# Kernel tuning notes

Hardware: AMD Instinct MI355X
Metric: run time of the kernel (lower is better)

## Reference

```python
import jax, jax.numpy as jnp
import numpy as np

BS, Q, K, NT = 16, 1500, 256, 150   # batch, queries, classes, GT per image (T = BS*NT)
COST_CLASS, COST_BBOX, COST_GIOU = 1.0, 5.0, 2.0
ALPHA, GAMMA, EPS = 0.25, 2.0, 1e-8


def box_cxcywh_to_xyxy(b):
    cx, cy, w, h = b[..., 0], b[..., 1], b[..., 2], b[..., 3]
    return jnp.stack([cx - 0.5 * w, cy - 0.5 * h, cx + 0.5 * w, cy + 0.5 * h], axis=-1)


def generalized_box_iou(boxes1, boxes2):
    # boxes in xyxy; boxes1: [N,4], boxes2: [M,4] -> [N,M]
    area1 = (boxes1[:, 2] - boxes1[:, 0]) * (boxes1[:, 3] - boxes1[:, 1])
    area2 = (boxes2[:, 2] - boxes2[:, 0]) * (boxes2[:, 3] - boxes2[:, 1])
    lt = jnp.maximum(boxes1[:, None, :2], boxes2[None, :, :2])
    rb = jnp.minimum(boxes1[:, None, 2:], boxes2[None, :, 2:])
    wh = jnp.clip(rb - lt, 0.0)
    inter = wh[..., 0] * wh[..., 1]
    union = area1[:, None] + area2[None, :] - inter
    iou = inter / union
    # smallest enclosing box
    lt_e = jnp.minimum(boxes1[:, None, :2], boxes2[None, :, :2])
    rb_e = jnp.maximum(boxes1[:, None, 2:], boxes2[None, :, 2:])
    wh_e = jnp.clip(rb_e - lt_e, 0.0)
    area_e = wh_e[..., 0] * wh_e[..., 1]
    return iou - (area_e - union) / area_e


def setup_inputs() -> dict:
    key = jax.random.key(0)
    k1, k2, k3, k4 = jax.random.split(key, 4)
    pred_logits = jax.random.normal(k1, (BS, Q, K), dtype=jnp.float32)
    pred_boxes = jax.random.uniform(k2, (BS, Q, 4), dtype=jnp.float32, minval=0.05, maxval=0.95)
    tgt_bbox = jax.random.uniform(k3, (BS * NT, 4), dtype=jnp.float32, minval=0.05, maxval=0.95)
    tgt_ids = jax.random.randint(k4, (BS * NT,), 0, K)
    return {"pred_logits": pred_logits, "pred_boxes": pred_boxes,
            "tgt_bbox": tgt_bbox, "tgt_ids": tgt_ids}


def reference(pred_logits, pred_boxes, tgt_bbox, tgt_ids):
    bs, nq, k = pred_logits.shape
    out_prob = jax.nn.sigmoid(pred_logits.reshape(bs * nq, k))   # [N, K]
    out_bbox = pred_boxes.reshape(bs * nq, 4)                    # [N, 4]

    # focal-style classification cost, gathered at target class columns
    neg_cost = (1.0 - ALPHA) * out_prob ** GAMMA * -jnp.log(1.0 - out_prob + EPS)
    pos_cost = ALPHA * (1.0 - out_prob) ** GAMMA * -jnp.log(out_prob + EPS)
    cost_class = (pos_cost - neg_cost)[:, tgt_ids]               # [N, T]

    # L1 box cost (cdist p=1)
    cost_bbox = jnp.sum(jnp.abs(out_bbox[:, None, :] - tgt_bbox[None, :, :]), axis=-1)

    # negative GIoU cost
    cost_giou = -generalized_box_iou(box_cxcywh_to_xyxy(out_bbox),
                                     box_cxcywh_to_xyxy(tgt_bbox))

    C = COST_BBOX * cost_bbox + COST_CLASS * cost_class + COST_GIOU * cost_giou
    return C.reshape(bs, nq, -1)                                  # [bs, Q, T]
```

## Files before the change

kernel.cpp:

```cpp
#include <hip/hip_runtime.h>
#include <hip/hip_fp16.h>
#include <cmath>


namespace {
constexpr int kBS = 16, kQ = 1500, kK = 256, kNT = 150;
constexpr int kT  = kBS * kNT;
constexpr int kN  = kBS * kQ;
constexpr int kQB = 16;
constexpr int kTT = 1024;
constexpr int kTiles = 3;
constexpr float kAlpha = 0.25f;
constexpr float kEps   = 1e-8f;
}

__global__ __launch_bounds__(256, 4)
void matcher_cost_kernel(const float* __restrict__ logits,
                         const float* __restrict__ pboxes,
                         const float* __restrict__ tboxes,
                         const int*   __restrict__ tids,
                         float* __restrict__ out)
{
    __shared__ float2 s_cxy[kTT];
    __shared__ float2 s_wh[kTT];
    __shared__ unsigned char s_cid[kTT];
    __shared__ __half s_fcl[kQB][kK];

    const int tid  = threadIdx.x;
    const int n0   = blockIdx.x * kQB;
    const int t0   = blockIdx.y * kTT;
    const int tsz  = min(kTT, kT - t0);

    const float4* tb4 = reinterpret_cast<const float4*>(tboxes);
    for (int j = tid; j < tsz; j += 256) {
        const float4 b = tb4[t0 + j];
        s_cxy[j] = make_float2(b.x, b.y);
        s_wh[j]  = make_float2(b.z, b.w);
        s_cid[j] = (unsigned char)tids[t0 + j];
    }

    for (int q = 0; q < kQB; ++q) {
        const float x   = logits[(n0 + q) * kK + tid];
        const float p   = __builtin_amdgcn_rcpf(1.0f + __expf(-x));
        const float omp = 1.0f - p;
        const float cc  = -kAlpha * omp * omp * __logf(p + kEps)
                        + (1.0f - kAlpha) * p * p * __logf(omp + kEps);
        s_fcl[q][tid] = __float2half(cc);
    }

    __syncthreads();

    for (int q = 0; q < kQB; ++q) {
        const int n = n0 + q;
        const float pcx = pboxes[n * 4 + 0];
        const float pcy = pboxes[n * 4 + 1];
        const float pw  = pboxes[n * 4 + 2];
        const float ph  = pboxes[n * 4 + 3];
        const float px1 = pcx - 0.5f * pw, px2 = pcx + 0.5f * pw;
        const float py1 = pcy - 0.5f * ph, py2 = pcy + 0.5f * ph;
        const float parea = pw * ph;
        float* __restrict__ row = out + (size_t)n * kT + t0;

        auto body = [&](int t) {
            const float2 cxy = s_cxy[t];
            const float2 wh  = s_wh[t];
            const float bcx = cxy.x, bcy = cxy.y, bw = wh.x, bh = wh.y;
            const float cc = __half2float(s_fcl[q][s_cid[t]]);
            const float cb = fabsf(pcx - bcx) + fabsf(pcy - bcy)
                           + fabsf(pw - bw)  + fabsf(ph - bh);
            const float tx1 = bcx - 0.5f * bw, tx2 = bcx + 0.5f * bw;
            const float ty1 = bcy - 0.5f * bh, ty2 = bcy + 0.5f * bh;
            const float ow = fminf(px2, tx2) - fmaxf(px1, tx1);
            const float oh = fminf(py2, ty2) - fmaxf(py1, ty1);
            const float iw = fmaxf(ow, 0.0f), ih = fmaxf(oh, 0.0f);
            const float ew = (pw + bw) - ow,  eh = (ph + bh) - oh;
            const float inter = iw * ih;
            const float uni   = parea + bw * bh - inter;
            const float earea = ew * eh;
            const float r    = __builtin_amdgcn_rcpf(uni * earea);
            const float frac = fmaf(uni, uni, inter * earea) * r;
            row[t] = fmaf(5.0f, cb, cc + 2.0f) - 2.0f * frac;
        };

        if (tsz == kTT) {
#pragma unroll
            for (int e = 0; e < 4; ++e) body(tid + 256 * e);
        } else {
            for (int t = tid; t < tsz; t += 256) body(t);
        }
    }
}

extern "C" void kernel_launch(void* const* d_in, const int* in_sizes, int n_in,
                              void* d_out, int out_size, void* d_ws, size_t ws_size,
                              hipStream_t stream) {
    const float* logits = (const float*)d_in[0];
    const float* pboxes = (const float*)d_in[1];
    const float* tboxes = (const float*)d_in[2];
    const int*   tids   = (const int*)d_in[3];
    float* out = (float*)d_out;

    dim3 grid(kN / kQB, kTiles);
    dim3 block(256);
    hipLaunchKernelGGL(matcher_cost_kernel, grid, block, 0, stream,
                       logits, pboxes, tboxes, tids, out);
}
```

Measured before the change: 274.5 us.

## Register-tile four targets per thread with float4 stores and transposed half2 class table

Each thread now keeps four consecutive target boxes and class ids in registers, with box corners and areas precomputed once, instead of staging them through shared memory. The class-cost table is transposed to [class][query-pair] as half2 with the +2 constant folded in, so one 8-byte LDS read covers four queries per target. Outputs are written as float4 vectors, and predicted boxes are read as float4. This cuts shared-memory traffic and per-element setup, at the cost of more registers and possible bank conflicts on the gathered table reads.

```diff
diff --git a/kernel.cpp b/kernel.cpp
--- a/kernel.cpp
+++ b/kernel.cpp
@@ -1,12 +1,10 @@
 #include <hip/hip_runtime.h>
 #include <hip/hip_fp16.h>
-#include <cmath>
 
 
 namespace {
 constexpr int kBS = 16, kQ = 1500, kK = 256, kNT = 150;
 constexpr int kT  = kBS * kNT;
-constexpr int kN  = kBS * kQ;
 constexpr int kQB = 16;
 constexpr int kTT = 1024;
 constexpr int kTiles = 3;
@@ -21,72 +19,97 @@
                          const int*   __restrict__ tids,
                          float* __restrict__ out)
 {
-    __shared__ float2 s_cxy[kTT];
-    __shared__ float2 s_wh[kTT];
-    __shared__ unsigned char s_cid[kTT];
-    __shared__ __half s_fcl[kQB][kK];
+    __shared__ __align__(16) __half2 s_fcl[kK][10];
 
-    const int tid  = threadIdx.x;
-    const int n0   = blockIdx.x * kQB;
-    const int t0   = blockIdx.y * kTT;
-    const int tsz  = min(kTT, kT - t0);
+    const int tid = threadIdx.x;
+    const int n0  = blockIdx.x * kQB;
+    const int t0  = blockIdx.y * kTT;
+    const int tsz = min(kTT, kT - t0);
 
-    const float4* tb4 = reinterpret_cast<const float4*>(tboxes);
-    for (int j = tid; j < tsz; j += 256) {
-        const float4 b = tb4[t0 + j];
-        s_cxy[j] = make_float2(b.x, b.y);
-        s_wh[j]  = make_float2(b.z, b.w);
-        s_cid[j] = (unsigned char)tids[t0 + j];
+    const int  tbase  = t0 + (tid << 2);
+    const bool active = (tid << 2) < tsz;
+    float4 tb[4];
+    int4 ci = make_int4(0, 0, 0, 0);
+    if (active) {
+        const float4* tb4 = reinterpret_cast<const float4*>(tboxes);
+        ci = *reinterpret_cast<const int4*>(tids + tbase);
+#pragma unroll
+        for (int e = 0; e < 4; ++e) tb[e] = tb4[tbase + e];
+    } else {
+#pragma unroll
+        for (int e = 0; e < 4; ++e) tb[e] = make_float4(0.f, 0.f, 1.f, 1.f);
     }
 
-    for (int q = 0; q < kQB; ++q) {
-        const float x   = logits[(n0 + q) * kK + tid];
-        const float p   = __builtin_amdgcn_rcpf(1.0f + __expf(-x));
-        const float omp = 1.0f - p;
-        const float cc  = -kAlpha * omp * omp * __logf(p + kEps)
-                        + (1.0f - kAlpha) * p * p * __logf(omp + kEps);
-        s_fcl[q][tid] = __float2half(cc);
+    {
+        const float* lrow = logits + n0 * kK + tid;
+#pragma unroll
+        for (int qp = 0; qp < kQB / 2; ++qp) {
+            float c[2];
+#pragma unroll
+            for (int j = 0; j < 2; ++j) {
+                const float x   = lrow[(2 * qp + j) * kK];
+                const float p   = __builtin_amdgcn_rcpf(1.0f + __expf(-x));
+                const float omp = 1.0f - p;
+                c[j] = -kAlpha * omp * omp * __logf(p + kEps)
+                     + (1.0f - kAlpha) * p * p * __logf(omp + kEps) + 2.0f;
+            }
+            s_fcl[tid][qp] = __floats2half2_rn(c[0], c[1]);
+        }
     }
 
     __syncthreads();
+    if (!active) return;
 
-    for (int q = 0; q < kQB; ++q) {
-        const int n = n0 + q;
-        const float pcx = pboxes[n * 4 + 0];
-        const float pcy = pboxes[n * 4 + 1];
-        const float pw  = pboxes[n * 4 + 2];
-        const float ph  = pboxes[n * 4 + 3];
-        const float px1 = pcx - 0.5f * pw, px2 = pcx + 0.5f * pw;
-        const float py1 = pcy - 0.5f * ph, py2 = pcy + 0.5f * ph;
-        const float parea = pw * ph;
-        float* __restrict__ row = out + (size_t)n * kT + t0;
+    int   cid[4];
+    float bcx[4], bcy[4], bw[4], bh[4], bx1[4], bx2[4], by1[4], by2[4], bar[4];
+    cid[0] = ci.x; cid[1] = ci.y; cid[2] = ci.z; cid[3] = ci.w;
+#pragma unroll
+    for (int e = 0; e < 4; ++e) {
+        bcx[e] = tb[e].x; bcy[e] = tb[e].y; bw[e] = tb[e].z; bh[e] = tb[e].w;
+        bx1[e] = bcx[e] - 0.5f * bw[e];  bx2[e] = bcx[e] + 0.5f * bw[e];
+        by1[e] = bcy[e] - 0.5f * bh[e];  by2[e] = bcy[e] + 0.5f * bh[e];
+        bar[e] = bw[e] * bh[e];
+    }
 
-        auto body = [&](int t) {
-            const float2 cxy = s_cxy[t];
-            const float2 wh  = s_wh[t];
-            const float bcx = cxy.x, bcy = cxy.y, bw = wh.x, bh = wh.y;
-            const float cc = __half2float(s_fcl[q][s_cid[t]]);
-            const float cb = fabsf(pcx - bcx) + fabsf(pcy - bcy)
-                           + fabsf(pw - bw)  + fabsf(ph - bh);
-            const float tx1 = bcx - 0.5f * bw, tx2 = bcx + 0.5f * bw;
-            const float ty1 = bcy - 0.5f * bh, ty2 = bcy + 0.5f * bh;
-            const float ow = fminf(px2, tx2) - fmaxf(px1, tx1);
-            const float oh = fminf(py2, ty2) - fmaxf(py1, ty1);
-            const float iw = fmaxf(ow, 0.0f), ih = fmaxf(oh, 0.0f);
-            const float ew = (pw + bw) - ow,  eh = (ph + bh) - oh;
-            const float inter = iw * ih;
-            const float uni   = parea + bw * bh - inter;
-            const float earea = ew * eh;
-            const float r    = __builtin_amdgcn_rcpf(uni * earea);
-            const float frac = fmaf(uni, uni, inter * earea) * r;
-            row[t] = fmaf(5.0f, cb, cc + 2.0f) - 2.0f * frac;
-        };
+    float* __restrict__ orow = out + (size_t)n0 * kT + tbase;
 
-        if (tsz == kTT) {
 #pragma unroll
-            for (int e = 0; e < 4; ++e) body(tid + 256 * e);
-        } else {
-            for (int t = tid; t < tsz; t += 256) body(t);
+    for (int qg = 0; qg < 4; ++qg) {
+        uint2 ccr[4];
+#pragma unroll
+        for (int e = 0; e < 4; ++e)
+            ccr[e] = *reinterpret_cast<const uint2*>(&s_fcl[cid[e]][qg * 2]);
+
+#pragma unroll
+        for (int qi = 0; qi < 4; ++qi) {
+            const int q = qg * 4 + qi;
+            const float4 pb = *reinterpret_cast<const float4*>(pboxes + (n0 + q) * 4);
+            const float pcx = pb.x, pcy = pb.y, pw = pb.z, ph = pb.w;
+            const float px1 = pcx - 0.5f * pw, px2 = pcx + 0.5f * pw;
+            const float py1 = pcy - 0.5f * ph, py2 = pcy + 0.5f * ph;
+            const float parea = pw * ph;
+
+            float res[4];
+#pragma unroll
+            for (int e = 0; e < 4; ++e) {
+                const unsigned u   = (qi < 2) ? ccr[e].x : ccr[e].y;
+                const __half2  h2  = *reinterpret_cast<const __half2*>(&u);
+                const float ccp2   = (qi & 1) ? __high2float(h2) : __low2float(h2);
+                const float cb = fabsf(pcx - bcx[e]) + fabsf(pcy - bcy[e])
+                               + fabsf(pw  - bw[e])  + fabsf(ph  - bh[e]);
+                const float ow = fminf(px2, bx2[e]) - fmaxf(px1, bx1[e]);
+                const float oh = fminf(py2, by2[e]) - fmaxf(py1, by1[e]);
+                const float iw = fmaxf(ow, 0.0f), ih = fmaxf(oh, 0.0f);
+                const float ew = (pw + bw[e]) - ow, eh = (ph + bh[e]) - oh;
+                const float inter = iw * ih;
+                const float uni   = (parea + bar[e]) - inter;
+                const float ear   = ew * eh;
+                const float rr   = __builtin_amdgcn_rcpf(uni * ear);
+                const float frac = fmaf(uni, uni, inter * ear) * rr;
+                res[e] = fmaf(5.0f, cb, ccp2) - 2.0f * frac;
+            }
+            *reinterpret_cast<float4*>(orow + (size_t)q * kT) =
+                make_float4(res[0], res[1], res[2], res[3]);
         }
     }
 }
@@ -100,7 +123,7 @@
     const int*   tids   = (const int*)d_in[3];
     float* out = (float*)d_out;
 
-    dim3 grid(kN / kQB, kTiles);
+    dim3 grid(kBS * kQ / kQB, kTiles);
     dim3 block(256);
     hipLaunchKernelGGL(matcher_cost_kernel, grid, block, 0, stream,
                        logits, pboxes, tboxes, tids, out);
```

New measurement: 269.6 us. Within noise of the previous version (-1.8%).

## Assign one query row per wavefront and write float4 outputs without block sync

Applied to the files above, without the earlier changes.

The kernel now gives each wavefront a whole query row across all 2400 targets instead of tiling 16 queries by 1024 targets per block. Target boxes and class ids are read straight from global/L1 rather than staged in shared memory. Each lane produces four consecutive outputs and stores them as a float4, and the per-row focal class cost is kept in fp32 in shared memory with no __syncthreads. This removes block-wide synchronisation and shared-memory staging and vectorises the dominant output stores, in exchange for repeated global reads of the target data and a larger grid of small blocks.

```diff
diff --git a/kernel.cpp b/kernel.cpp
--- a/kernel.cpp
+++ b/kernel.cpp
@@ -1,15 +1,10 @@
 #include <hip/hip_runtime.h>
-#include <hip/hip_fp16.h>
-#include <cmath>
-
 
 namespace {
 constexpr int kBS = 16, kQ = 1500, kK = 256, kNT = 150;
-constexpr int kT  = kBS * kNT;
-constexpr int kN  = kBS * kQ;
-constexpr int kQB = 16;
-constexpr int kTT = 1024;
-constexpr int kTiles = 3;
+constexpr int kT   = kBS * kNT;
+constexpr int kN   = kBS * kQ;
+constexpr int kQPB = 4;
 constexpr float kAlpha = 0.25f;
 constexpr float kEps   = 1e-8f;
 }
@@ -21,74 +16,65 @@
                          const int*   __restrict__ tids,
                          float* __restrict__ out)
 {
-    __shared__ float2 s_cxy[kTT];
-    __shared__ float2 s_wh[kTT];
-    __shared__ unsigned char s_cid[kTT];
-    __shared__ __half s_fcl[kQB][kK];
+    __shared__ float s_fcl[kQPB][kK];
 
     const int tid  = threadIdx.x;
-    const int n0   = blockIdx.x * kQB;
-    const int t0   = blockIdx.y * kTT;
-    const int tsz  = min(kTT, kT - t0);
+    const int wv   = tid >> 6;
+    const int lane = tid & 63;
+    const int n    = blockIdx.x * kQPB + wv;
 
-    const float4* tb4 = reinterpret_cast<const float4*>(tboxes);
-    for (int j = tid; j < tsz; j += 256) {
-        const float4 b = tb4[t0 + j];
-        s_cxy[j] = make_float2(b.x, b.y);
-        s_wh[j]  = make_float2(b.z, b.w);
-        s_cid[j] = (unsigned char)tids[t0 + j];
+    const float4 pb = *reinterpret_cast<const float4*>(pboxes + (size_t)n * 4);
+
+    const float* lrow = logits + (size_t)n * kK;
+#pragma unroll
+    for (int j = 0; j < kK / 64; ++j) {
+        const int   c   = lane + 64 * j;
+        const float x   = lrow[c];
+        const float p   = __builtin_amdgcn_rcpf(1.0f + __expf(-x));
+        const float omp = 1.0f - p;
+        s_fcl[wv][c] = -kAlpha * omp * omp * __logf(p + kEps)
+                     + (1.0f - kAlpha) * p * p * __logf(omp + kEps) + 2.0f;
     }
 
-    for (int q = 0; q < kQB; ++q) {
-        const float x   = logits[(n0 + q) * kK + tid];
-        const float p   = __builtin_amdgcn_rcpf(1.0f + __expf(-x));
-        const float omp = 1.0f - p;
-        const float cc  = -kAlpha * omp * omp * __logf(p + kEps)
-                        + (1.0f - kAlpha) * p * p * __logf(omp + kEps);
-        s_fcl[q][tid] = __float2half(cc);
-    }
+    const float pcx = pb.x, pcy = pb.y, pw = pb.z, ph = pb.w;
+    const float px1 = pcx - 0.5f * pw, px2 = pcx + 0.5f * pw;
+    const float py1 = pcy - 0.5f * ph, py2 = pcy + 0.5f * ph;
+    const float parea = pw * ph;
 
-    __syncthreads();
+    const float4* __restrict__ tb4  = reinterpret_cast<const float4*>(tboxes);
+    float* __restrict__        orow = out + (size_t)n * kT;
 
-    for (int q = 0; q < kQB; ++q) {
-        const int n = n0 + q;
-        const float pcx = pboxes[n * 4 + 0];
-        const float pcy = pboxes[n * 4 + 1];
-        const float pw  = pboxes[n * 4 + 2];
-        const float ph  = pboxes[n * 4 + 3];
-        const float px1 = pcx - 0.5f * pw, px2 = pcx + 0.5f * pw;
-        const float py1 = pcy - 0.5f * ph, py2 = pcy + 0.5f * ph;
-        const float parea = pw * ph;
-        float* __restrict__ row = out + (size_t)n * kT + t0;
-
-        auto body = [&](int t) {
-            const float2 cxy = s_cxy[t];
-            const float2 wh  = s_wh[t];
-            const float bcx = cxy.x, bcy = cxy.y, bw = wh.x, bh = wh.y;
-            const float cc = __half2float(s_fcl[q][s_cid[t]]);
+    auto group4 = [&](int t) {
+        const int4 ci = *reinterpret_cast<const int4*>(tids + t);
+        float4 res;
+        float* rp = &res.x;
+        const int cid[4] = {ci.x, ci.y, ci.z, ci.w};
+#pragma unroll
+        for (int e = 0; e < 4; ++e) {
+            const float4 b  = tb4[t + e];
+            const float  cc = s_fcl[wv][cid[e]];
+            const float bcx = b.x, bcy = b.y, bw = b.z, bh = b.w;
             const float cb = fabsf(pcx - bcx) + fabsf(pcy - bcy)
                            + fabsf(pw - bw)  + fabsf(ph - bh);
-            const float tx1 = bcx - 0.5f * bw, tx2 = bcx + 0.5f * bw;
-            const float ty1 = bcy - 0.5f * bh, ty2 = bcy + 0.5f * bh;
-            const float ow = fminf(px2, tx2) - fmaxf(px1, tx1);
-            const float oh = fminf(py2, ty2) - fmaxf(py1, ty1);
+            const float bx1 = fmaf(-0.5f, bw, bcx), bx2 = fmaf(0.5f, bw, bcx);
+            const float by1 = fmaf(-0.5f, bh, bcy), by2 = fmaf(0.5f, bh, bcy);
+            const float ow = fminf(px2, bx2) - fmaxf(px1, bx1);
+            const float oh = fminf(py2, by2) - fmaxf(py1, by1);
             const float iw = fmaxf(ow, 0.0f), ih = fmaxf(oh, 0.0f);
             const float ew = (pw + bw) - ow,  eh = (ph + bh) - oh;
             const float inter = iw * ih;
-            const float uni   = parea + bw * bh - inter;
-            const float earea = ew * eh;
-            const float r    = __builtin_amdgcn_rcpf(uni * earea);
-            const float frac = fmaf(uni, uni, inter * earea) * r;
-            row[t] = fmaf(5.0f, cb, cc + 2.0f) - 2.0f * frac;
-        };
+            const float uni   = fmaf(bw, bh, parea) - inter;
+            const float ear   = ew * eh;
+            const float rr   = __builtin_amdgcn_rcpf(uni * ear);
+            const float frac = fmaf(uni, uni, inter * ear) * rr;
+            rp[e] = fmaf(-2.0f, frac, fmaf(5.0f, cb, cc));
+        }
+        *reinterpret_cast<float4*>(orow + t) = res;
+    };
 
-        if (tsz == kTT) {
-#pragma unroll
-            for (int e = 0; e < 4; ++e) body(tid + 256 * e);
-        } else {
-            for (int t = tid; t < tsz; t += 256) body(t);
-        }
-    }
+#pragma unroll 3
+    for (int it = 0; it < 9; ++it) group4(it * 256 + lane * 4);
+    if (lane < 24) group4(2304 + lane * 4);
 }
 
 extern "C" void kernel_launch(void* const* d_in, const int* in_sizes, int n_in,
@@ -100,7 +86,7 @@
     const int*   tids   = (const int*)d_in[3];
     float* out = (float*)d_out;
 
-    dim3 grid(kN / kQB, kTiles);
+    dim3 grid(kN / kQPB);
     dim3 block(256);
     hipLaunchKernelGGL(matcher_cost_kernel, grid, block, 0, stream,
                        logits, pboxes, tboxes, tids, out);
```

Measured after the change: 304.0 us. +10.7%, slower.
